# Performance work log

Measured on AMD Instinct MI355X. Metric: run time of the kernel, lower is better.

Reference implementation:

```python
import jax, jax.numpy as jnp
import numpy as np

B = 32768
D_IN = 512      # input_dim == dict_dim (forced by the STE add)
HID = 512       # hard-coded hidden width of linear1
D = 512         # dict_dim / embedding_dim
P = 8           # per_factor_dict_size: number of codebooks / MLP branches
K = 10          # num_factor: codebook size (rows per embedding table)
COMMIT = 0.25


def setup_inputs() -> dict:
    key = jax.random.key(0)
    ks = jax.random.split(key, 7)
    s1 = 1.0 / np.sqrt(D_IN)
    s2 = 1.0 / np.sqrt(HID)
    return {
        "inputs": jax.random.normal(ks[0], (B, D_IN), jnp.float32),
        "W1": jax.random.uniform(ks[1], (P, HID, D_IN), jnp.float32, -s1, s1),
        "b1": jax.random.uniform(ks[2], (P, HID), jnp.float32, -s1, s1),
        "W2": jax.random.uniform(ks[3], (P, D, HID), jnp.float32, -s2, s2),
        "b2": jax.random.uniform(ks[4], (P, D), jnp.float32, -s2, s2),
        # embedding init: uniform(-1/num_factor, 1/num_factor)
        "E": jax.random.uniform(ks[5], (P, K, D), jnp.float32, -1.0 / K, 1.0 / K),
        "label_gen": jax.random.randint(ks[6], (B,), 0, K, jnp.int64),
    }


def reference(inputs, W1, b1, W2, b2, E, label_gen):
    sg = jax.lax.stop_gradient
    # P parallel 2-layer MLPs: [P, B, D]
    h = jax.nn.relu(jnp.einsum("bd,phd->pbh", inputs, W1) + b1[:, None, :])
    z = jnp.einsum("pbh,peh->pbe", h, W2) + b2[:, None, :]
    # squared-distance expansion per codebook: [P, B, K]
    distances = (
        jnp.sum(z * z, axis=-1, keepdims=True)
        + jnp.sum(E * E, axis=-1)[:, None, :]
        - 2.0 * jnp.einsum("pbd,pkd->pbk", z, E)
    )
    ave_distances = jnp.mean(distances, axis=0)          # [B, K]
    idx = jnp.argmin(ave_distances, axis=1)              # [B]
    # one-hot @ E[p] then mean over p == mean codebook gathered at idx
    Emean = jnp.mean(E, axis=0)                          # [K, D]
    vq = Emean[idx]                                      # [B, D]
    vq_z = inputs + sg(vq - inputs)                      # straight-through
    # all_vq_z[j] = mean_p E[p, j]; losses vs every code row: [K, B]
    diff1 = Emean[:, None, :] - sg(inputs)[None, :, :]   # [K, B, D]
    diff2 = sg(Emean)[:, None, :] - inputs[None, :, :]
    all_vq_loss = jnp.sum(diff1 * diff1, axis=-1) + COMMIT * jnp.sum(diff2 * diff2, axis=-1)
    all_vq_z = inputs[None, :, :] + sg(Emean[:, None, :] - inputs[None, :, :])  # [K, B, D]
    changed_vq_z = Emean[label_gen]                      # [B, D]
    return (vq_z, distances, all_vq_z, all_vq_loss, changed_vq_z)
```

## Files before the change

kernel.cpp:

```cpp
#include <hip/hip_runtime.h>
#include <stdint.h>

typedef _Float16 f16;
typedef _Float16 f16x8 __attribute__((ext_vector_type(8)));
typedef float f32x4 __attribute__((ext_vector_type(4)));

#define B_ROWS 32768
#define DIM 512
#define NP 8
#define NK 10

typedef __attribute__((address_space(3))) unsigned int lds_u32;
typedef __attribute__((address_space(1))) const unsigned int gbl_u32;

__device__ __forceinline__ void gload_lds16(const void* g, void* l) {
  __builtin_amdgcn_global_load_lds((gbl_u32*)(uintptr_t)g, (lds_u32*)(uintptr_t)l, 16, 0, 0);
}


__global__ void prep_split(const float* __restrict__ X, f16* __restrict__ Xh,
                           f16* __restrict__ Xl, const float* __restrict__ W1,
                           f16* __restrict__ W1h, f16* __restrict__ W1l,
                           const float* __restrict__ W2, f16* __restrict__ W2h) {
  int bid = blockIdx.x, tid = threadIdx.x;
  if (bid < 2048) {
    for (int i = bid * 256 + tid; i < 16777216; i += 2048 * 256) {
      float v = X[i];
      f16 h = (f16)v;
      Xh[i] = h;
      Xl[i] = (f16)(v - (float)h);
    }
  } else if (bid < 2560) {
    for (int i = (bid - 2048) * 256 + tid; i < 2097152; i += 512 * 256) {
      float v = W1[i];
      f16 h = (f16)v;
      W1h[i] = h;
      W1l[i] = (f16)(v - (float)h);
    }
  } else {
    for (int i = (bid - 2560) * 256 + tid; i < 2097152; i += 512 * 256) {
      W2h[i] = (f16)W2[i];
    }
  }
}


__global__ void enorm2(const float* __restrict__ E, float* __restrict__ Emean,
                       float* __restrict__ E2, float* __restrict__ E2m) {
  int bid = blockIdx.x;
  int lane = threadIdx.x;
  if (bid < 80) {
    const float* src = E + (size_t)bid * DIM;
    float s = 0.f;
    for (int i = lane; i < DIM; i += 64) {
      float v = src[i];
      s = fmaf(v, v, s);
    }
#pragma unroll
    for (int m = 1; m < 64; m <<= 1) s += __shfl_xor(s, m, 64);
    if (lane == 0) E2[bid] = s;
  } else {
    int k = bid - 80;
    float acc = 0.f;
    for (int i = lane; i < DIM; i += 64) {
      float s = 0.f;
#pragma unroll
      for (int p = 0; p < NP; ++p) s += E[p * NK * DIM + k * DIM + i];
      s *= 0.125f;
      Emean[k * DIM + i] = s;
      acc = fmaf(s, s, acc);
    }
#pragma unroll
    for (int m = 1; m < 64; m <<= 1) acc += __shfl_xor(acc, m, 64);
    if (lane == 0) E2m[k] = acc;
  }
}


__global__ __launch_bounds__(512) void etilde_kernel(const float* __restrict__ W2,
                                                     const float* __restrict__ b2,
                                                     const float* __restrict__ E,
                                                     f16* __restrict__ EimgH,
                                                     f16* __restrict__ EimgL,
                                                     float* __restrict__ c_) {
  const int p = blockIdx.x / NK, k = blockIdx.x % NK;
  const int h = threadIdx.x;
  __shared__ float Er[512];
  __shared__ float red[8];
  Er[h] = E[((size_t)p * NK + k) * DIM + h];
  __syncthreads();
  const float* Wp = W2 + (size_t)p * DIM * DIM;
  float s = 0.f;
#pragma unroll 8
  for (int d = 0; d < DIM; ++d) s = fmaf(Wp[(size_t)d * DIM + h], Er[d], s);
  int ei = p * 8320 + k * 520 + h;
  f16 hi = (f16)s;
  EimgH[ei] = hi;
  EimgL[ei] = (f16)(s - (float)hi);
  if (h < 8) {
    int pi = p * 8320 + k * 520 + 512 + h;
    EimgH[pi] = (f16)0.f;
    EimgL[pi] = (f16)0.f;
  }
  if (k == 0) {
    for (int j = h; j < 6 * 520; j += 512) {
      int pi = p * 8320 + 10 * 520 + j;
      EimgH[pi] = (f16)0.f;
      EimgL[pi] = (f16)0.f;
    }
  }
  float t = b2[p * DIM + h] * Er[h];
#pragma unroll
  for (int m = 1; m < 64; m <<= 1) t += __shfl_xor(t, m, 64);
  if ((h & 63) == 0) red[h >> 6] = t;
  __syncthreads();
  if (h == 0) {
    float cc = 0.f;
#pragma unroll
    for (int i = 0; i < 8; ++i) cc += red[i];
    c_[p * NK + k] = cc;
  }
}


template <int EPI, int NBN, int NPROD, int GRP>
__global__ __launch_bounds__(256) void gemmA(
    const f16* __restrict__ Ah_, const f16* __restrict__ Al_, int lda, int apitch,
    const f16* __restrict__ Bh_, const f16* __restrict__ Bl_, int bpitch,
    const float* __restrict__ bias_, int bias_pitch,
    f16* __restrict__ Oh, f16* __restrict__ Ol, int ldo,
    float* __restrict__ part2) {
  __shared__ f16 smem[32768];
  const int tid = threadIdx.x;
  const int lane = tid & 63;
  const int wave = tid >> 6;
  const int wr = wave >> 1, wc = wave & 1;
  const int p = blockIdx.z;

  const int q8 = gridDim.x >> 3;
  const int bid = blockIdx.x;
  const int swz = (bid & 7) * q8 + (bid >> 3);
  const int band = swz / (GRP * NBN);
  const int r_ = swz % (GRP * NBN);
  const int bm = band * GRP + (r_ % GRP);
  const int bn = r_ / GRP;
  const int m0 = bm * 128, n0 = bn * 128;

  const f16* Ahp = Ah_ + (size_t)p * apitch;
  const f16* Alp = Al_ + (size_t)p * apitch;
  const f16* Bhp = Bh_ + (size_t)p * bpitch;
  const f16* Blp = Bl_ + (size_t)p * bpitch;

  const int NT = (NPROD == 3) ? 24 : 8;

  f32x4 acc[4][4] = {};

  auto stage = [&](int buf, int t) {
    const f16* As;
    const f16* Bs;
    int k0;
    if (NPROD == 3) {
      int pr = t % 3;
      As = (pr == 2) ? Alp : Ahp;
      Bs = (pr == 1) ? Blp : Bhp;
      k0 = (t / 3) * 64;
    } else {
      As = Ahp;
      Bs = Bhp;
      k0 = t * 64;
    }
    f16* sA = smem + buf * 16384;
    f16* sB = sA + 8192;
#pragma unroll
    for (int j = 0; j < 4; ++j) {
      int r = j * 32 + (tid >> 3);
      int c = ((tid & 7) ^ (r & 7)) * 8;
      gload_lds16(As + (size_t)(m0 + r) * lda + k0 + c, sA + j * 2048 + tid * 8);
      gload_lds16(Bs + (size_t)(n0 + r) * 512 + k0 + c, sB + j * 2048 + tid * 8);
    }
  };

  stage(0, 0);
  __syncthreads();

  const int g = lane >> 4, rl = lane & 15;

  for (int s = 0; s < NT; ++s) {
    int nx = s + 1;
    if (nx < NT) stage(nx & 1, nx);
    const char* sA = (const char*)(smem + (s & 1) * 16384);
    const char* sB = sA + 16384;
    f16x8 af[4][2], bf[4][2];
#pragma unroll
    for (int i = 0; i < 4; ++i) {
      int ra = wr * 64 + i * 16 + rl;
      int rb = wc * 64 + i * 16 + rl;
#pragma unroll
      for (int kk = 0; kk < 2; ++kk) {
        int cb = kk * 64 + g * 16;
        af[i][kk] = *(const f16x8*)(sA + ra * 128 + (cb ^ ((ra & 7) << 4)));
        bf[i][kk] = *(const f16x8*)(sB + rb * 128 + (cb ^ ((rb & 7) << 4)));
      }
    }
#pragma unroll
    for (int i = 0; i < 4; ++i)
#pragma unroll
      for (int jn = 0; jn < 4; ++jn)
#pragma unroll
        for (int kk = 0; kk < 2; ++kk)
          acc[i][jn] = __builtin_amdgcn_mfma_f32_16x16x32_f16(af[i][kk], bf[jn][kk], acc[i][jn], 0, 0, 0);
    __syncthreads();
  }

  if (EPI == 0) {
#pragma unroll
    for (int jn = 0; jn < 4; ++jn) {
      int cg = n0 + wc * 64 + jn * 16 + rl;
      float bv = bias_[cg];
#pragma unroll
      for (int i = 0; i < 4; ++i) {
        int r0 = m0 + wr * 64 + i * 16 + g * 4;
#pragma unroll
        for (int r = 0; r < 4; ++r) {
          float z = acc[i][jn][r] + bv;
          z = fmaxf(z, 0.f);
          f16 h = (f16)z;
          size_t off = (size_t)(r0 + r) * ldo + cg;
          Oh[off] = h;
          Ol[off] = (f16)(z - (float)h);
        }
      }
    }
  } else {
    const float* bp = bias_ + (size_t)p * bias_pitch;
    float bvals[4];
#pragma unroll
    for (int jn = 0; jn < 4; ++jn) bvals[jn] = bp[n0 + wc * 64 + jn * 16 + rl];
    const int ch = bn * 2 + wc;
    float* pb = part2 + (size_t)(p * 8 + ch) * B_ROWS;
#pragma unroll
    for (int i = 0; i < 4; ++i) {
#pragma unroll
      for (int r = 0; r < 4; ++r) {
        float q = 0.f;
#pragma unroll
        for (int jn = 0; jn < 4; ++jn) {
          float z = acc[i][jn][r] + bvals[jn];
          q = fmaf(z, z, q);
        }
#pragma unroll
        for (int m = 1; m < 16; m <<= 1) q += __shfl_xor(q, m, 64);
        if (rl == 0) pb[m0 + wr * 64 + i * 16 + g * 4 + r] = q;
      }
    }
  }
}


__global__ __launch_bounds__(256) void dots_mfma(const f16* __restrict__ Hh,
                                                 const f16* __restrict__ Hl,
                                                 const f16* __restrict__ EimgH,
                                                 const f16* __restrict__ EimgL,
                                                 const float* __restrict__ c_,
                                                 float* __restrict__ gout) {
  __shared__ f16 sH[8192];
  __shared__ f16 sL[8192];
  __shared__ f16 sEh[16 * 520];
  __shared__ f16 sEl[16 * 520];
  const int tid = threadIdx.x;
  const int lane = tid & 63, wave = tid >> 6;
  const int p = blockIdx.y;
  const int r0 = blockIdx.x * 128;
  {
    const uint32_t* ih = (const uint32_t*)(EimgH + (size_t)p * 16 * 520);
    const uint32_t* il = (const uint32_t*)(EimgL + (size_t)p * 16 * 520);
    uint32_t* oh = (uint32_t*)sEh;
    uint32_t* ol = (uint32_t*)sEl;
    for (int i = tid; i < 16 * 520 / 2; i += 256) {
      oh[i] = ih[i];
      ol[i] = il[i];
    }
  }
  const int gq = lane >> 4, rl = lane & 15;
  f32x4 acc[2] = {};
  for (int t = 0; t < 8; ++t) {
    __syncthreads();
#pragma unroll
    for (int j = 0; j < 4; ++j) {
      int r = j * 32 + (tid >> 3);
      int c = ((tid & 7) ^ (r & 7)) * 8;
      gload_lds16(Hh + (size_t)(r0 + r) * 4096 + p * DIM + t * 64 + c, sH + j * 2048 + tid * 8);
      gload_lds16(Hl + (size_t)(r0 + r) * 4096 + p * DIM + t * 64 + c, sL + j * 2048 + tid * 8);
    }
    __syncthreads();
    const char* bh = (const char*)sH;
    const char* bl = (const char*)sL;
    const char* eh = (const char*)sEh;
    const char* el = (const char*)sEl;
    f16x8 ah[2][2], al[2][2], beh[2], bel[2];
#pragma unroll
    for (int mf = 0; mf < 2; ++mf) {
      int ra = wave * 32 + mf * 16 + rl;
#pragma unroll
      for (int kk = 0; kk < 2; ++kk) {
        int cb = kk * 64 + gq * 16;
        ah[mf][kk] = *(const f16x8*)(bh + ra * 128 + (cb ^ ((ra & 7) << 4)));
        al[mf][kk] = *(const f16x8*)(bl + ra * 128 + (cb ^ ((ra & 7) << 4)));
      }
    }
#pragma unroll
    for (int kk = 0; kk < 2; ++kk) {
      int cb = t * 128 + kk * 64 + gq * 16;
      beh[kk] = *(const f16x8*)(eh + rl * 1040 + cb);
      bel[kk] = *(const f16x8*)(el + rl * 1040 + cb);
    }
#pragma unroll
    for (int mf = 0; mf < 2; ++mf)
#pragma unroll
      for (int kk = 0; kk < 2; ++kk) {
        acc[mf] = __builtin_amdgcn_mfma_f32_16x16x32_f16(ah[mf][kk], beh[kk], acc[mf], 0, 0, 0);
        acc[mf] = __builtin_amdgcn_mfma_f32_16x16x32_f16(ah[mf][kk], bel[kk], acc[mf], 0, 0, 0);
        acc[mf] = __builtin_amdgcn_mfma_f32_16x16x32_f16(al[mf][kk], beh[kk], acc[mf], 0, 0, 0);
      }
  }
  if (rl < NK) {
    float cv = c_[p * NK + rl];
#pragma unroll
    for (int mf = 0; mf < 2; ++mf)
#pragma unroll
      for (int r = 0; r < 4; ++r) {
        int row = r0 + wave * 32 + mf * 16 + gq * 4 + r;
        gout[((size_t)p * B_ROWS + row) * NK + rl] = acc[mf][r] + cv;
      }
  }
}


__global__ __launch_bounds__(256) void final_kernel(
    const float* __restrict__ X, const float* __restrict__ part2,
    float* __restrict__ gdist, const float* __restrict__ E2,
    const float* __restrict__ Emean, const float* __restrict__ E2m,
    const int* __restrict__ label, float* __restrict__ vq_z,
    float* __restrict__ avz, float* __restrict__ loss, float* __restrict__ changed) {
  __shared__ float Em[NK * DIM];
  __shared__ float e2s[NK];
  const int tid = threadIdx.x;
  for (int i = tid; i < NK * DIM; i += 256) Em[i] = Emean[i];
  if (tid < NK) e2s[tid] = E2m[tid];
  __syncthreads();

  const int b0 = blockIdx.x * 16;
  {
    const float4* Em4 = (const float4*)Em;
    float4* avz4 = (float4*)avz;
    if (blockIdx.x < 256) {
      for (int it = 0; it < 80; ++it) {
        int idx = it * 256 + tid;
        int d4 = idx & 127, row = (idx >> 7) & 15, k = idx >> 11;
        if (k == 8) continue;
        avz4[(((size_t)k * B_ROWS + b0 + row) << 7) + d4] = Em4[k * 128 + d4];
      }
    } else {
      for (int it = 0; it < 80; ++it) {
        int idx = it * 256 + tid;
        int d4 = idx & 127, row = (idx >> 7) & 15, k = idx >> 11;
        avz4[(((size_t)k * B_ROWS + b0 + row) << 7) + d4] = Em4[k * 128 + d4];
      }
    }
  }

  const int lane = tid & 63, wave = tid >> 6;
  const int pl = lane & 7, kh = lane >> 3;
  for (int rr = 0; rr < 4; ++rr) {
    int b = b0 + wave * 4 + rr;
    float zq = part2[(size_t)(pl * 8 + kh) * B_ROWS + b];
    zq += __shfl_xor(zq, 8, 64);
    zq += __shfl_xor(zq, 16, 64);
    zq += __shfl_xor(zq, 32, 64);
    float g0 = gdist[((size_t)pl * B_ROWS + b) * NK + kh];
    float g1 = (lane < 16) ? gdist[((size_t)pl * B_ROWS + b) * NK + 8 + kh] : 0.f;
    float dv0 = zq + E2[pl * NK + kh] - 2.f * g0;
    float dv1 = zq + E2[pl * NK + 8 + kh] - 2.f * g1;
    gdist[((size_t)pl * B_ROWS + b) * NK + kh] = dv0;
    if (lane < 16) gdist[((size_t)pl * B_ROWS + b) * NK + 8 + kh] = dv1;
    float v0 = dv0, v1 = (lane < 16) ? dv1 : 0.f;
#pragma unroll
    for (int m = 1; m < 8; m <<= 1) {
      v0 += __shfl_xor(v0, m, 64);
      v1 += __shfl_xor(v1, m, 64);
    }
    float a[NK];
#pragma unroll
    for (int k = 0; k < 8; ++k) a[k] = __shfl(v0, k * 8, 64);
    a[8] = __shfl(v1, 0, 64);
    a[9] = __shfl(v1, 8, 64);
    int idx = 0;
    float mn = a[0];
#pragma unroll
    for (int k = 1; k < NK; ++k) {
      if (a[k] < mn) { mn = a[k]; idx = k; }
    }
    const float* xr = X + (size_t)b * DIM;
    float sx = 0.f, dx[NK] = {};
#pragma unroll
    for (int j = 0; j < 8; ++j) {
      float x = xr[j * 64 + lane];
      sx = fmaf(x, x, sx);
#pragma unroll
      for (int k = 0; k < NK; ++k) dx[k] = fmaf(x, Em[k * DIM + j * 64 + lane], dx[k]);
    }
#pragma unroll
    for (int m = 1; m < 64; m <<= 1) {
      sx += __shfl_xor(sx, m, 64);
#pragma unroll
      for (int k = 0; k < NK; ++k) dx[k] += __shfl_xor(dx[k], m, 64);
    }
    if (lane == 0) {
#pragma unroll
      for (int k = 0; k < NK; ++k)
        loss[(size_t)k * B_ROWS + b] = 1.25f * (sx - 2.f * dx[k] + e2s[k]);
    }
    int lab = label[b];
#pragma unroll
    for (int j = 0; j < 8; ++j) {
      int c = j * 64 + lane;
      vq_z[(size_t)b * DIM + c] = Em[idx * DIM + c];
      changed[(size_t)b * DIM + c] = Em[lab * DIM + c];
    }
  }
}


__global__ void bcast_rest(const float* __restrict__ Emean, float4* __restrict__ avz4) {
  const float4* Em4 = (const float4*)Emean;
  int tid = blockIdx.x * 256 + threadIdx.x;
  for (int it = 0; it < 32; ++it) {
    int idx = tid + it * 16384;
    int b = idx >> 7, d4 = idx & 127;
    avz4[((size_t)(8 * B_ROWS + b) << 7) + d4] = Em4[8 * 128 + d4];
  }
}


extern "C" void kernel_launch(void* const* d_in, const int* in_sizes, int n_in,
                              void* d_out, int out_size, void* d_ws, size_t ws_size,
                              hipStream_t stream) {
  const float* X = (const float*)d_in[0];
  const float* W1 = (const float*)d_in[1];
  const float* b1 = (const float*)d_in[2];
  const float* W2 = (const float*)d_in[3];
  const float* b2 = (const float*)d_in[4];
  const float* E = (const float*)d_in[5];
  const int* lab = (const int*)d_in[6];
  float* out = (float*)d_out;

  float* vq_z = out;
  float* dist = out + 16777216;
  float* avz = out + 16777216 + 2621440;
  float* loss = avz + 167772160;
  float* chg = loss + 327680;

  f16* Xh = (f16*)vq_z;
  f16* Xl = Xh + 16777216;
  f16* Hh = (f16*)avz;
  f16* Hl = Hh + 134217728;
  float* part2 = avz + 134217728;

  char* w = (char*)d_ws;
  f16* W1h = (f16*)w; w += 4194304;
  f16* W1l = (f16*)w; w += 4194304;
  f16* W2h = (f16*)w; w += 4194304;
  float* Emean = (float*)w; w += NK * DIM * 4;
  float* E2 = (float*)w; w += 512;
  float* E2m = (float*)w; w += 256;
  float* c_ = (float*)w; w += 512;
  f16* EimgH = (f16*)w; w += NP * 16 * 520 * 2;
  f16* EimgL = (f16*)w; w += NP * 16 * 520 * 2;

  prep_split<<<3072, 256, 0, stream>>>(X, Xh, Xl, W1, W1h, W1l, W2, W2h);
  enorm2<<<90, 64, 0, stream>>>(E, Emean, E2, E2m);
  etilde_kernel<<<80, 512, 0, stream>>>(W2, b2, E, EimgH, EimgL, c_);

  gemmA<0, 32, 3, 8><<<dim3(8192, 1, 1), 256, 0, stream>>>(
      Xh, Xl, 512, 0, W1h, W1l, 0, b1, 0, Hh, Hl, 4096, nullptr);
  gemmA<1, 4, 1, 1><<<dim3(1024, 1, NP), 256, 0, stream>>>(
      Hh, Hh, 4096, 512, W2h, W2h, 262144, b2, 512, nullptr, nullptr, 0, part2);

  dots_mfma<<<dim3(256, NP), 256, 0, stream>>>(Hh, Hl, EimgH, EimgL, c_, dist);
  final_kernel<<<2048, 256, 0, stream>>>(X, part2, dist, E2, Emean, E2m, lab,
                                         vq_z, avz, loss, chg);
  bcast_rest<<<64, 256, 0, stream>>>(Emean, (float4*)avz);
}
```

Measured before the change: 1.100 ms.

## Vectorize prep split and double-buffer dots_mfma with smaller row tiles

```diff
diff --git a/kernel.cpp b/kernel.cpp
--- a/kernel.cpp
+++ b/kernel.cpp
@@ -2,6 +2,7 @@
 #include <stdint.h>
 
 typedef _Float16 f16;
+typedef _Float16 f16x4 __attribute__((ext_vector_type(4)));
 typedef _Float16 f16x8 __attribute__((ext_vector_type(8)));
 typedef float f32x4 __attribute__((ext_vector_type(4)));
 
@@ -18,28 +19,34 @@
 }
 
 
-__global__ void prep_split(const float* __restrict__ X, f16* __restrict__ Xh,
-                           f16* __restrict__ Xl, const float* __restrict__ W1,
-                           f16* __restrict__ W1h, f16* __restrict__ W1l,
-                           const float* __restrict__ W2, f16* __restrict__ W2h) {
+__global__ void prep_split(const float4* __restrict__ X4, f16x4* __restrict__ Xh4,
+                           f16x4* __restrict__ Xl4, const float4* __restrict__ W14,
+                           f16x4* __restrict__ W1h4, f16x4* __restrict__ W1l4,
+                           const float4* __restrict__ W24, f16x4* __restrict__ W2h4) {
   int bid = blockIdx.x, tid = threadIdx.x;
-  if (bid < 2048) {
-    for (int i = bid * 256 + tid; i < 16777216; i += 2048 * 256) {
-      float v = X[i];
-      f16 h = (f16)v;
-      Xh[i] = h;
-      Xl[i] = (f16)(v - (float)h);
-    }
-  } else if (bid < 2560) {
-    for (int i = (bid - 2048) * 256 + tid; i < 2097152; i += 512 * 256) {
-      float v = W1[i];
-      f16 h = (f16)v;
-      W1h[i] = h;
-      W1l[i] = (f16)(v - (float)h);
+  if (bid < 1024) {
+    for (int i = bid * 256 + tid; i < 4194304; i += 1024 * 256) {
+      float4 v = X4[i];
+      f16x4 h = {(f16)v.x, (f16)v.y, (f16)v.z, (f16)v.w};
+      f16x4 l = {(f16)(v.x - (float)h[0]), (f16)(v.y - (float)h[1]),
+                 (f16)(v.z - (float)h[2]), (f16)(v.w - (float)h[3])};
+      Xh4[i] = h;
+      Xl4[i] = l;
+    }
+  } else if (bid < 1152) {
+    for (int i = (bid - 1024) * 256 + tid; i < 524288; i += 128 * 256) {
+      float4 v = W14[i];
+      f16x4 h = {(f16)v.x, (f16)v.y, (f16)v.z, (f16)v.w};
+      f16x4 l = {(f16)(v.x - (float)h[0]), (f16)(v.y - (float)h[1]),
+                 (f16)(v.z - (float)h[2]), (f16)(v.w - (float)h[3])};
+      W1h4[i] = h;
+      W1l4[i] = l;
     }
   } else {
-    for (int i = (bid - 2560) * 256 + tid; i < 2097152; i += 512 * 256) {
-      W2h[i] = (f16)W2[i];
+    for (int i = (bid - 1152) * 256 + tid; i < 524288; i += 128 * 256) {
+      float4 v = W24[i];
+      f16x4 h = {(f16)v.x, (f16)v.y, (f16)v.z, (f16)v.w};
+      W2h4[i] = h;
     }
   }
 }
@@ -263,14 +270,14 @@
                                                  const f16* __restrict__ EimgL,
                                                  const float* __restrict__ c_,
                                                  float* __restrict__ gout) {
-  __shared__ f16 sH[8192];
-  __shared__ f16 sL[8192];
+  __shared__ f16 sH[2][4096];
+  __shared__ f16 sL[2][4096];
   __shared__ f16 sEh[16 * 520];
   __shared__ f16 sEl[16 * 520];
   const int tid = threadIdx.x;
   const int lane = tid & 63, wave = tid >> 6;
   const int p = blockIdx.y;
-  const int r0 = blockIdx.x * 128;
+  const int r0 = blockIdx.x * 64;
   {
     const uint32_t* ih = (const uint32_t*)(EimgH + (size_t)p * 16 * 520);
     const uint32_t* il = (const uint32_t*)(EimgL + (size_t)p * 16 * 520);
@@ -282,56 +289,52 @@
     }
   }
   const int gq = lane >> 4, rl = lane & 15;
-  f32x4 acc[2] = {};
+
+  auto stageT = [&](int buf, int t) {
+#pragma unroll
+    for (int rnd = 0; rnd < 2; ++rnd) {
+      int w = rnd * 256 + tid;
+      int r = w >> 3;
+      int c = ((w & 7) ^ (r & 7)) * 8;
+      gload_lds16(Hh + (size_t)(r0 + r) * 4096 + p * DIM + t * 64 + c, &sH[buf][(size_t)w * 8]);
+      gload_lds16(Hl + (size_t)(r0 + r) * 4096 + p * DIM + t * 64 + c, &sL[buf][(size_t)w * 8]);
+    }
+  };
+
+  f32x4 acc = {};
+  stageT(0, 0);
+  __syncthreads();
+
   for (int t = 0; t < 8; ++t) {
+    if (t < 7) stageT((t + 1) & 1, t + 1);
+    const char* bh = (const char*)sH[t & 1];
+    const char* bl = (const char*)sL[t & 1];
+    const int ra = wave * 16 + rl;
+    f16x8 ah[2], al[2], beh[2], bel[2];
+#pragma unroll
+    for (int kk = 0; kk < 2; ++kk) {
+      int cb = kk * 64 + gq * 16;
+      ah[kk] = *(const f16x8*)(bh + ra * 128 + (cb ^ ((ra & 7) << 4)));
+      al[kk] = *(const f16x8*)(bl + ra * 128 + (cb ^ ((ra & 7) << 4)));
+      int ce = t * 128 + kk * 64 + gq * 16;
+      beh[kk] = *(const f16x8*)((const char*)sEh + rl * 1040 + ce);
+      bel[kk] = *(const f16x8*)((const char*)sEl + rl * 1040 + ce);
+    }
+#pragma unroll
+    for (int kk = 0; kk < 2; ++kk) {
+      acc = __builtin_amdgcn_mfma_f32_16x16x32_f16(ah[kk], beh[kk], acc, 0, 0, 0);
+      acc = __builtin_amdgcn_mfma_f32_16x16x32_f16(ah[kk], bel[kk], acc, 0, 0, 0);
+      acc = __builtin_amdgcn_mfma_f32_16x16x32_f16(al[kk], beh[kk], acc, 0, 0, 0);
+    }
     __syncthreads();
-#pragma unroll
-    for (int j = 0; j < 4; ++j) {
-      int r = j * 32 + (tid >> 3);
-      int c = ((tid & 7) ^ (r & 7)) * 8;
-      gload_lds16(Hh + (size_t)(r0 + r) * 4096 + p * DIM + t * 64 + c, sH + j * 2048 + tid * 8);
-      gload_lds16(Hl + (size_t)(r0 + r) * 4096 + p * DIM + t * 64 + c, sL + j * 2048 + tid * 8);
-    }
-    __syncthreads();
-    const char* bh = (const char*)sH;
-    const char* bl = (const char*)sL;
-    const char* eh = (const char*)sEh;
-    const char* el = (const char*)sEl;
-    f16x8 ah[2][2], al[2][2], beh[2], bel[2];
-#pragma unroll
-    for (int mf = 0; mf < 2; ++mf) {
-      int ra = wave * 32 + mf * 16 + rl;
-#pragma unroll
-      for (int kk = 0; kk < 2; ++kk) {
-        int cb = kk * 64 + gq * 16;
-        ah[mf][kk] = *(const f16x8*)(bh + ra * 128 + (cb ^ ((ra & 7) << 4)));
-        al[mf][kk] = *(const f16x8*)(bl + ra * 128 + (cb ^ ((ra & 7) << 4)));
-      }
-    }
-#pragma unroll
-    for (int kk = 0; kk < 2; ++kk) {
-      int cb = t * 128 + kk * 64 + gq * 16;
-      beh[kk] = *(const f16x8*)(eh + rl * 1040 + cb);
-      bel[kk] = *(const f16x8*)(el + rl * 1040 + cb);
-    }
-#pragma unroll
-    for (int mf = 0; mf < 2; ++mf)
-#pragma unroll
-      for (int kk = 0; kk < 2; ++kk) {
-        acc[mf] = __builtin_amdgcn_mfma_f32_16x16x32_f16(ah[mf][kk], beh[kk], acc[mf], 0, 0, 0);
-        acc[mf] = __builtin_amdgcn_mfma_f32_16x16x32_f16(ah[mf][kk], bel[kk], acc[mf], 0, 0, 0);
-        acc[mf] = __builtin_amdgcn_mfma_f32_16x16x32_f16(al[mf][kk], beh[kk], acc[mf], 0, 0, 0);
-      }
   }
   if (rl < NK) {
     float cv = c_[p * NK + rl];
 #pragma unroll
-    for (int mf = 0; mf < 2; ++mf)
-#pragma unroll
-      for (int r = 0; r < 4; ++r) {
-        int row = r0 + wave * 32 + mf * 16 + gq * 4 + r;
-        gout[((size_t)p * B_ROWS + row) * NK + rl] = acc[mf][r] + cv;
-      }
+    for (int r = 0; r < 4; ++r) {
+      int row = r0 + wave * 16 + gq * 4 + r;
+      gout[((size_t)p * B_ROWS + row) * NK + rl] = acc[r] + cv;
+    }
   }
 }
 
@@ -477,7 +480,9 @@
   f16* EimgH = (f16*)w; w += NP * 16 * 520 * 2;
   f16* EimgL = (f16*)w; w += NP * 16 * 520 * 2;
 
-  prep_split<<<3072, 256, 0, stream>>>(X, Xh, Xl, W1, W1h, W1l, W2, W2h);
+  prep_split<<<1280, 256, 0, stream>>>((const float4*)X, (f16x4*)Xh, (f16x4*)Xl,
+                                       (const float4*)W1, (f16x4*)W1h, (f16x4*)W1l,
+                                       (const float4*)W2, (f16x4*)W2h);
   enorm2<<<90, 64, 0, stream>>>(E, Emean, E2, E2m);
   etilde_kernel<<<80, 512, 0, stream>>>(W2, b2, E, EimgH, EimgL, c_);
 
@@ -486,7 +491,7 @@
   gemmA<1, 4, 1, 1><<<dim3(1024, 1, NP), 256, 0, stream>>>(
       Hh, Hh, 4096, 512, W2h, W2h, 262144, b2, 512, nullptr, nullptr, 0, part2);
 
-  dots_mfma<<<dim3(256, NP), 256, 0, stream>>>(Hh, Hl, EimgH, EimgL, c_, dist);
+  dots_mfma<<<dim3(512, NP), 256, 0, stream>>>(Hh, Hl, EimgH, EimgL, c_, dist);
   final_kernel<<<2048, 256, 0, stream>>>(X, part2, dist, E2, Emean, E2m, lab,
                                          vq_z, avz, loss, chg);
   bcast_rest<<<64, 256, 0, stream>>>(Emean, (float4*)avz);
```

Measured after the change: 1.110 ms. Within noise of the previous version (+1.0%).
